# Optimization experiments

Measured on AMD Instinct MI355X. Metric: run time of the kernel, lower is better.

## Reference

```python
import jax, jax.numpy as jnp
import numpy as np

B, T, D, L, N_MELS, MAX_R = 128, 1024, 256, 512, 80, 20

def setup_inputs() -> dict:
    key = jax.random.key(0)
    ks = jax.random.split(key, 40)
    s = 0.05
    inp = {
        'encoder_seq': jax.random.normal(ks[0], (B, T, D), jnp.float32),
        'encoder_seq_proj': jax.random.normal(ks[1], (B, T, D), jnp.float32),
        'prenet_in': jax.random.normal(ks[2], (B, N_MELS), jnp.float32),
        'attn_hidden': jax.random.normal(ks[3], (B, D), jnp.float32),
        'rnn1_hidden': jax.random.normal(ks[4], (B, L), jnp.float32),
        'rnn2_hidden': jax.random.normal(ks[5], (B, L), jnp.float32),
        'rnn1_cell': jax.random.normal(ks[6], (B, L), jnp.float32),
        'rnn2_cell': jax.random.normal(ks[7], (B, L), jnp.float32),
        'context_vec': jax.random.normal(ks[8], (B, D), jnp.float32),
        # PreNet
        'fc1_W': jax.random.normal(ks[9], (256, N_MELS), jnp.float32) * s,
        'fc1_b': jnp.zeros((256,), jnp.float32),
        'fc2_W': jax.random.normal(ks[10], (128, 256), jnp.float32) * s,
        'fc2_b': jnp.zeros((128,), jnp.float32),
        # Attention
        'attn_W': jax.random.normal(ks[11], (D, D), jnp.float32) * s,
        'attn_v': jax.random.normal(ks[12], (1, D), jnp.float32) * s,
        # GRUCell: input size D + D//2 = 384
        'gru_Wih': jax.random.normal(ks[13], (3 * D, D + D // 2), jnp.float32) * s,
        'gru_Whh': jax.random.normal(ks[14], (3 * D, D), jnp.float32) * s,
        'gru_bih': jnp.zeros((3 * D,), jnp.float32),
        'gru_bhh': jnp.zeros((3 * D,), jnp.float32),
        # rnn_input Linear: 2*D -> L
        'rnn_in_W': jax.random.normal(ks[15], (L, 2 * D), jnp.float32) * s,
        'rnn_in_b': jnp.zeros((L,), jnp.float32),
        # LSTMCell 1
        'l1_Wih': jax.random.normal(ks[16], (4 * L, L), jnp.float32) * s,
        'l1_Whh': jax.random.normal(ks[17], (4 * L, L), jnp.float32) * s,
        'l1_bih': jnp.zeros((4 * L,), jnp.float32),
        'l1_bhh': jnp.zeros((4 * L,), jnp.float32),
        # LSTMCell 2
        'l2_Wih': jax.random.normal(ks[18], (4 * L, L), jnp.float32) * s,
        'l2_Whh': jax.random.normal(ks[19], (4 * L, L), jnp.float32) * s,
        'l2_bih': jnp.zeros((4 * L,), jnp.float32),
        'l2_bhh': jnp.zeros((4 * L,), jnp.float32),
        # mel projection (no bias)
        'mel_W': jax.random.normal(ks[20], (N_MELS * MAX_R, L), jnp.float32) * s,
        'r': 2,
    }
    return inp


def _lstm_cell(x, h, c, Wih, Whh, bih, bhh):
    g = x @ Wih.T + bih + h @ Whh.T + bhh
    i, f, gg, o = jnp.split(g, 4, axis=-1)
    c_new = jax.nn.sigmoid(f) * c + jax.nn.sigmoid(i) * jnp.tanh(gg)
    h_new = jax.nn.sigmoid(o) * jnp.tanh(c_new)
    return h_new, c_new


def reference(encoder_seq, encoder_seq_proj, prenet_in, attn_hidden, rnn1_hidden,
              rnn2_hidden, rnn1_cell, rnn2_cell, context_vec,
              fc1_W, fc1_b, fc2_W, fc2_b, attn_W, attn_v,
              gru_Wih, gru_Whh, gru_bih, gru_bhh, rnn_in_W, rnn_in_b,
              l1_Wih, l1_Whh, l1_bih, l1_bhh, l2_Wih, l2_Whh, l2_bih, l2_bhh,
              mel_W, r):
    # PreNet (eval mode: dropout identity)
    p = jax.nn.relu(prenet_in @ fc1_W.T + fc1_b)
    p = jax.nn.relu(p @ fc2_W.T + fc2_b)  # [B, D//2]

    # GRUCell (torch semantics)
    x_in = jnp.concatenate([context_vec, p], axis=-1)  # [B, D + D//2]
    gi = x_in @ gru_Wih.T + gru_bih
    gh = attn_hidden @ gru_Whh.T + gru_bhh
    i_r, i_z, i_n = jnp.split(gi, 3, axis=-1)
    h_r, h_z, h_n = jnp.split(gh, 3, axis=-1)
    rg = jax.nn.sigmoid(i_r + h_r)
    zg = jax.nn.sigmoid(i_z + h_z)
    ng = jnp.tanh(i_n + rg * h_n)
    attn_h = (1.0 - zg) * ng + zg * attn_hidden  # [B, D]

    # Bahdanau attention, softmax over time (dim=1)
    q = attn_h @ attn_W.T  # [B, D]
    u = jnp.tanh(encoder_seq_proj + q[:, None, :]) @ attn_v.T  # [B, T, 1]
    scores = jax.nn.softmax(u, axis=1)
    scores_t = jnp.swapaxes(scores, 1, 2)  # [B, 1, T]
    context = jnp.matmul(scores_t, encoder_seq)[:, 0, :]  # [B, D]

    x = jnp.concatenate([context, attn_h], axis=1) @ rnn_in_W.T + rnn_in_b  # [B, L]

    rnn1_h, rnn1_c = _lstm_cell(x, rnn1_hidden, rnn1_cell, l1_Wih, l1_Whh, l1_bih, l1_bhh)
    x = x + rnn1_h
    rnn2_h, rnn2_c = _lstm_cell(x, rnn2_hidden, rnn2_cell, l2_Wih, l2_Whh, l2_bih, l2_bhh)
    x = x + rnn2_h

    mels = (x @ mel_W.T).reshape(x.shape[0], N_MELS, MAX_R)[:, :, :r]
    return (mels, scores_t, attn_h, rnn1_h, rnn2_h, rnn1_c, rnn2_c, context)
```

## Files before the change

kernel.cpp:

```cpp
#include <hip/hip_runtime.h>
#include <math.h>

#define B_   128
#define T_   1024
#define D_   256
#define L_   512

__device__ __forceinline__ float sigmoidf_(float x) {
    return 1.f / (1.f + __expf(-x));
}
__device__ __forceinline__ float tanhf_(float x) {
    x = fminf(fmaxf(x, -15.f), 15.f);
    float e = __expf(2.f * x);
    return (e - 1.f) / (e + 1.f);
}
__device__ __forceinline__ float tanh_fast(float x) {
    float e = __expf(2.f * x);
    return 1.f - 2.f * __builtin_amdgcn_rcpf(e + 1.f);
}
__device__ __forceinline__ float waveReduceSum(float v) {
    #pragma unroll
    for (int o = 32; o > 0; o >>= 1) v += __shfl_xor(v, o, 64);
    return v;
}
__device__ __forceinline__ float waveReduceMax(float v) {
    #pragma unroll
    for (int o = 32; o > 0; o >>= 1) v = fmaxf(v, __shfl_xor(v, o, 64));
    return v;
}

__global__ __launch_bounds__(256) void k1a_prenet(
    const float* __restrict__ prenet_in,
    const float* __restrict__ fc1_W, const float* __restrict__ fc1_b,
    const float* __restrict__ fc2_W, const float* __restrict__ fc2_b,
    float* __restrict__ p2_out)
{
    const int b = blockIdx.x, t = threadIdx.x;
    __shared__ __align__(16) float pin[80];
    __shared__ __align__(16) float p1[256];

    if (t < 80) pin[t] = prenet_in[b * 80 + t];
    __syncthreads();

    {
        float a = fc1_b[t];
        const float4* w  = (const float4*)(fc1_W + t * 80);
        const float4* xv = (const float4*)pin;
        #pragma unroll
        for (int k = 0; k < 20; k++) {
            float4 wv = w[k], v = xv[k];
            a += v.x * wv.x + v.y * wv.y + v.z * wv.z + v.w * wv.w;
        }
        p1[t] = fmaxf(a, 0.f);
    }
    __syncthreads();

    if (t < 128) {
        float a = fc2_b[t];
        const float4* w  = (const float4*)(fc2_W + t * 256);
        const float4* xv = (const float4*)p1;
        #pragma unroll 8
        for (int k = 0; k < 64; k++) {
            float4 wv = w[k], v = xv[k];
            a += v.x * wv.x + v.y * wv.y + v.z * wv.z + v.w * wv.w;
        }
        p2_out[b * 128 + t] = fmaxf(a, 0.f);
    }
}

__global__ __launch_bounds__(256) void k1b_gru_gemv(
    const float* __restrict__ context_vec, const float* __restrict__ p2,
    const float* __restrict__ attn_hidden,
    const float* __restrict__ gru_Wih, const float* __restrict__ gru_Whh,
    const float* __restrict__ gru_bih, const float* __restrict__ gru_bhh,
    float* __restrict__ gi_out, float* __restrict__ gh_out)
{
    const int t = threadIdx.x;
    const int j = blockIdx.x * 256 + t;
    const int b0 = blockIdx.y * 2;

    __shared__ __align__(16) float xs[2][384];
    __shared__ __align__(16) float hs[2][256];

    for (int i = t; i < 768; i += 256) {
        int bb = i / 384, k = i % 384;
        xs[bb][k] = (k < 256) ? context_vec[(b0 + bb) * 256 + k]
                              : p2[(b0 + bb) * 128 + (k - 256)];
    }
    for (int i = t; i < 512; i += 256) {
        hs[i / 256][i % 256] = attn_hidden[(b0 + i / 256) * 256 + (i % 256)];
    }
    __syncthreads();

    {
        float a0 = gru_bih[j], a1 = a0;
        const float4* w  = (const float4*)(gru_Wih + (size_t)j * 384);
        const float4* x0 = (const float4*)xs[0];
        const float4* x1 = (const float4*)xs[1];
        #pragma unroll 8
        for (int k = 0; k < 96; k++) {
            float4 wv = w[k], v0 = x0[k], v1 = x1[k];
            a0 += v0.x * wv.x + v0.y * wv.y + v0.z * wv.z + v0.w * wv.w;
            a1 += v1.x * wv.x + v1.y * wv.y + v1.z * wv.z + v1.w * wv.w;
        }
        gi_out[(size_t)(b0 + 0) * 768 + j] = a0;
        gi_out[(size_t)(b0 + 1) * 768 + j] = a1;
    }
    {
        float a0 = gru_bhh[j], a1 = a0;
        const float4* w  = (const float4*)(gru_Whh + (size_t)j * 256);
        const float4* x0 = (const float4*)hs[0];
        const float4* x1 = (const float4*)hs[1];
        #pragma unroll 8
        for (int k = 0; k < 64; k++) {
            float4 wv = w[k], v0 = x0[k], v1 = x1[k];
            a0 += v0.x * wv.x + v0.y * wv.y + v0.z * wv.z + v0.w * wv.w;
            a1 += v1.x * wv.x + v1.y * wv.y + v1.z * wv.z + v1.w * wv.w;
        }
        gh_out[(size_t)(b0 + 0) * 768 + j] = a0;
        gh_out[(size_t)(b0 + 1) * 768 + j] = a1;
    }
}

__global__ __launch_bounds__(256) void k1c_gates_q(
    const float* __restrict__ gi, const float* __restrict__ gh,
    const float* __restrict__ attn_hidden, const float* __restrict__ attn_W,
    float* __restrict__ attn_h_out, float* __restrict__ q_out)
{
    const int b = blockIdx.x, t = threadIdx.x;
    __shared__ __align__(16) float ahn[256];

    {
        float hp = attn_hidden[b * 256 + t];
        float rg = sigmoidf_(gi[(size_t)b * 768 + t]       + gh[(size_t)b * 768 + t]);
        float zg = sigmoidf_(gi[(size_t)b * 768 + 256 + t] + gh[(size_t)b * 768 + 256 + t]);
        float ng = tanhf_(gi[(size_t)b * 768 + 512 + t] + rg * gh[(size_t)b * 768 + 512 + t]);
        float h  = (1.f - zg) * ng + zg * hp;
        ahn[t] = h;
        attn_h_out[b * 256 + t] = h;
    }
    __syncthreads();

    {
        float a = 0.f;
        const float4* w  = (const float4*)(attn_W + (size_t)t * 256);
        const float4* xv = (const float4*)ahn;
        #pragma unroll 8
        for (int k = 0; k < 64; k++) {
            float4 wv = w[k], v = xv[k];
            a += v.x * wv.x + v.y * wv.y + v.z * wv.z + v.w * wv.w;
        }
        q_out[b * 256 + t] = a;
    }
}

__global__ __launch_bounds__(256) void ka_attn(
    const float* __restrict__ enc_proj, const float* __restrict__ enc,
    const float* __restrict__ q, const float* __restrict__ v,
    float* __restrict__ u_out, float* __restrict__ ctx_part,
    float* __restrict__ m_part, float* __restrict__ s_part)
{
    const int b     = blockIdx.x >> 4;
    const int chunk = blockIdx.x & 15;
    const int tid   = threadIdx.x;
    const int lane  = tid & 63;
    const int wv    = tid >> 6;
    const int g     = lane >> 4;
    const int gl    = lane & 15;

    __shared__ float ul[64];
    __shared__ float el[64];
    __shared__ __align__(16) float4 red[4][64];

    const int t0 = chunk * 64;

    float4 qv[4], vv[4];
    #pragma unroll
    for (int c = 0; c < 4; c++) {
        qv[c] = ((const float4*)(q + b * 256))[c * 16 + gl];
        vv[c] = ((const float4*)v)[c * 16 + gl];
    }

    const float* ebase = enc_proj + ((size_t)(b * T_ + t0)) * 256;
    #pragma unroll
    for (int pass = 0; pass < 4; pass++) {
        const int t = wv * 16 + pass * 4 + g;
        const float4* row = (const float4*)(ebase + (size_t)t * 256);
        float s = 0.f;
        #pragma unroll
        for (int c = 0; c < 4; c++) {
            float4 pj = row[c * 16 + gl];
            s += tanh_fast(pj.x + qv[c].x) * vv[c].x
               + tanh_fast(pj.y + qv[c].y) * vv[c].y
               + tanh_fast(pj.z + qv[c].z) * vv[c].z
               + tanh_fast(pj.w + qv[c].w) * vv[c].w;
        }
        s += __shfl_xor(s, 1, 64);
        s += __shfl_xor(s, 2, 64);
        s += __shfl_xor(s, 4, 64);
        s += __shfl_xor(s, 8, 64);
        if (gl == 0) ul[t] = s;
    }
    __syncthreads();

    if (wv == 0) {
        float x = ul[lane];
        u_out[b * T_ + t0 + lane] = x;
        float mx = waveReduceMax(x);
        float e = __expf(x - mx);
        el[lane] = e;
        float ss = waveReduceSum(e);
        if (lane == 0) {
            m_part[b * 16 + chunk] = mx;
            s_part[b * 16 + chunk] = ss;
        }
    }
    __syncthreads();

    const float4* base2 = (const float4*)(enc + ((size_t)(b * T_ + t0)) * 256);
    float4 acc0 = {0.f, 0.f, 0.f, 0.f}, acc1 = {0.f, 0.f, 0.f, 0.f};
    #pragma unroll
    for (int i = 0; i < 16; i += 2) {
        int t = wv * 16 + i;
        float e0 = el[t], e1 = el[t + 1];
        float4 v0 = base2[(size_t)t * 64 + lane];
        float4 v1 = base2[(size_t)(t + 1) * 64 + lane];
        acc0.x += e0 * v0.x; acc0.y += e0 * v0.y; acc0.z += e0 * v0.z; acc0.w += e0 * v0.w;
        acc1.x += e1 * v1.x; acc1.y += e1 * v1.y; acc1.z += e1 * v1.z; acc1.w += e1 * v1.w;
    }
    acc0.x += acc1.x; acc0.y += acc1.y; acc0.z += acc1.z; acc0.w += acc1.w;
    red[wv][lane] = acc0;
    __syncthreads();
    if (tid < 64) {
        float4 s = red[0][tid];
        float4 a1 = red[1][tid], a2 = red[2][tid], a3 = red[3][tid];
        s.x += a1.x + a2.x + a3.x;
        s.y += a1.y + a2.y + a3.y;
        s.z += a1.z + a2.z + a3.z;
        s.w += a1.w + a2.w + a3.w;
        ((float4*)ctx_part)[(size_t)(b * 16 + chunk) * 64 + tid] = s;
    }
}

__global__ __launch_bounds__(256) void kb_combine(
    const float* __restrict__ u, const float* __restrict__ m_part,
    const float* __restrict__ s_part, const float* __restrict__ ctx_part,
    const float* __restrict__ attn_h,
    float* __restrict__ scores_out, float* __restrict__ ctx_out,
    float* __restrict__ concat1)
{
    const int b = blockIdx.x, tid = threadIdx.x;
    __shared__ float msh[16], ssh[16];
    if (tid < 16) {
        msh[tid] = m_part[b * 16 + tid];
        ssh[tid] = s_part[b * 16 + tid];
    }
    __syncthreads();

    float M = msh[0];
    #pragma unroll
    for (int c = 1; c < 16; c++) M = fmaxf(M, msh[c]);
    float S = 0.f;
    #pragma unroll
    for (int c = 0; c < 16; c++) S += ssh[c] * __expf(msh[c] - M);
    float invS = 1.f / S;

    {
        float a = 0.f;
        #pragma unroll
        for (int c = 0; c < 16; c++)
            a += ctx_part[(size_t)(b * 16 + c) * 256 + tid] * __expf(msh[c] - M);
        a *= invS;
        ctx_out[b * 256 + tid] = a;
        concat1[b * 512 + tid] = a;
        concat1[b * 512 + 256 + tid] = attn_h[b * 256 + tid];
    }

    #pragma unroll
    for (int i = 0; i < 4; i++) {
        int t = i * 256 + tid;
        scores_out[b * T_ + t] = __expf(u[b * T_ + t] - M) * invS;
    }
}

__global__ __launch_bounds__(256) void gemm512_splitk(
    const float* __restrict__ A1, const float* __restrict__ W1,
    const float* __restrict__ A2, const float* __restrict__ W2,
    float* __restrict__ part, int N, int ksPerSeg)
{
    const int n0 = blockIdx.x * 64, m0 = blockIdx.y * 64;
    const int seg = blockIdx.z / ksPerSeg, ls = blockIdx.z % ksPerSeg;
    const int KSZ = 512 / ksPerSeg;
    const float* A = seg ? A2 : A1;
    const float* W = seg ? W2 : W1;
    const int k0 = ls * KSZ;

    __shared__ __align__(16) float As[32][68];
    __shared__ __align__(16) float Ws[32][68];

    const int tid = threadIdx.x;
    const int tm = tid & 15, tn = tid >> 4;
    const int rs = tid >> 3, qs = tid & 7;

    float acc[4][4] = {};

    for (int kt = 0; kt < KSZ; kt += 32) {
        #pragma unroll
        for (int it = 0; it < 2; it++) {
            int r = rs + it * 32;
            float4 av = *(const float4*)(A + (size_t)(m0 + r) * 512 + k0 + kt + qs * 4);
            As[qs * 4 + 0][r] = av.x; As[qs * 4 + 1][r] = av.y;
            As[qs * 4 + 2][r] = av.z; As[qs * 4 + 3][r] = av.w;
            float4 wv = *(const float4*)(W + (size_t)(n0 + r) * 512 + k0 + kt + qs * 4);
            Ws[qs * 4 + 0][r] = wv.x; Ws[qs * 4 + 1][r] = wv.y;
            Ws[qs * 4 + 2][r] = wv.z; Ws[qs * 4 + 3][r] = wv.w;
        }
        __syncthreads();
        #pragma unroll
        for (int kk = 0; kk < 32; kk++) {
            float4 a = *(const float4*)&As[kk][tm * 4];
            float4 w = *(const float4*)&Ws[kk][tn * 4];
            acc[0][0] += a.x * w.x; acc[0][1] += a.x * w.y; acc[0][2] += a.x * w.z; acc[0][3] += a.x * w.w;
            acc[1][0] += a.y * w.x; acc[1][1] += a.y * w.y; acc[1][2] += a.y * w.z; acc[1][3] += a.y * w.w;
            acc[2][0] += a.z * w.x; acc[2][1] += a.z * w.y; acc[2][2] += a.z * w.z; acc[2][3] += a.z * w.w;
            acc[3][0] += a.w * w.x; acc[3][1] += a.w * w.y; acc[3][2] += a.w * w.z; acc[3][3] += a.w * w.w;
        }
        __syncthreads();
    }

    float* pb = part + ((size_t)blockIdx.z * 128 + m0) * N + n0;
    #pragma unroll
    for (int i = 0; i < 4; i++) {
        float4 o = {acc[i][0], acc[i][1], acc[i][2], acc[i][3]};
        *(float4*)(pb + (size_t)(tm * 4 + i) * N + tn * 4) = o;
    }
}

__global__ __launch_bounds__(256) void e_rnn(
    const float* __restrict__ part, const float* __restrict__ bias,
    float* __restrict__ x)
{
    const int idx = blockIdx.x * 256 + threadIdx.x;
    const int n = idx & 511;
    float a = bias[n];
    #pragma unroll
    for (int z = 0; z < 4; z++) a += part[(size_t)z * 65536 + idx];
    x[idx] = a;
}

__global__ __launch_bounds__(256) void e_lstm(
    const float* __restrict__ part,
    const float* __restrict__ bih, const float* __restrict__ bhh,
    const float* __restrict__ c_prev, const float* __restrict__ x_prev,
    float* __restrict__ h_out, float* __restrict__ c_out, float* __restrict__ x_new)
{
    const int idx = blockIdx.x * 256 + threadIdx.x;
    const int bb = idx >> 9, j = idx & 511;
    float gi = bih[j] + bhh[j];
    float gf = bih[512 + j] + bhh[512 + j];
    float gg = bih[1024 + j] + bhh[1024 + j];
    float go = bih[1536 + j] + bhh[1536 + j];
    #pragma unroll
    for (int z = 0; z < 4; z++) {
        const float* p = part + ((size_t)z * 128 + bb) * 2048;
        gi += p[j]; gf += p[512 + j]; gg += p[1024 + j]; go += p[1536 + j];
    }
    float c = sigmoidf_(gf) * c_prev[idx] + sigmoidf_(gi) * tanhf_(gg);
    float h = sigmoidf_(go) * tanhf_(c);
    h_out[idx] = h;
    c_out[idx] = c;
    x_new[idx] = x_prev[idx] + h;
}

__global__ __launch_bounds__(512) void e_lstm2_mel(
    const float* __restrict__ part,
    const float* __restrict__ bih, const float* __restrict__ bhh,
    const float* __restrict__ c_prev, const float* __restrict__ x_prev,
    const float* __restrict__ mel_W, const int* __restrict__ r_ptr,
    float* __restrict__ h_out, float* __restrict__ c_out,
    float* __restrict__ mels)
{
    const int b = blockIdx.x, j = threadIdx.x;
    __shared__ __align__(16) float xs[512];

    const int idx = b * 512 + j;
    float gi = bih[j] + bhh[j];
    float gf = bih[512 + j] + bhh[512 + j];
    float gg = bih[1024 + j] + bhh[1024 + j];
    float go = bih[1536 + j] + bhh[1536 + j];
    #pragma unroll
    for (int z = 0; z < 4; z++) {
        const float* p = part + ((size_t)z * 128 + b) * 2048;
        gi += p[j]; gf += p[512 + j]; gg += p[1024 + j]; go += p[1536 + j];
    }
    float c = sigmoidf_(gf) * c_prev[idx] + sigmoidf_(gi) * tanhf_(gg);
    float h = sigmoidf_(go) * tanhf_(c);
    h_out[idx] = h;
    c_out[idx] = c;
    xs[j] = x_prev[idx] + h;
    __syncthreads();

    const int r = r_ptr[0];
    const int tot = 80 * r;
    for (int n = j; n < tot; n += 512) {
        int m = n / r, rr = n % r;
        const float4* w  = (const float4*)(mel_W + (size_t)(m * 20 + rr) * 512);
        const float4* xv = (const float4*)xs;
        float a = 0.f;
        #pragma unroll 8
        for (int k = 0; k < 128; k++) {
            float4 wv = w[k], vv = xv[k];
            a += wv.x * vv.x + wv.y * vv.y + wv.z * vv.z + wv.w * vv.w;
        }
        mels[(size_t)b * tot + n] = a;
    }
}

extern "C" void kernel_launch(void* const* d_in, const int* in_sizes, int n_in,
                              void* d_out, int out_size, void* d_ws, size_t ws_size,
                              hipStream_t stream)
{
    const float* enc   = (const float*)d_in[0];
    const float* encp  = (const float*)d_in[1];
    const float* pre   = (const float*)d_in[2];
    const float* ah_in = (const float*)d_in[3];
    const float* r1h   = (const float*)d_in[4];
    const float* r2h   = (const float*)d_in[5];
    const float* r1c   = (const float*)d_in[6];
    const float* r2c   = (const float*)d_in[7];
    const float* cvec  = (const float*)d_in[8];
    const float* fc1W  = (const float*)d_in[9];
    const float* fc1b  = (const float*)d_in[10];
    const float* fc2W  = (const float*)d_in[11];
    const float* fc2b  = (const float*)d_in[12];
    const float* attnW = (const float*)d_in[13];
    const float* attnv = (const float*)d_in[14];
    const float* gWih  = (const float*)d_in[15];
    const float* gWhh  = (const float*)d_in[16];
    const float* gbih  = (const float*)d_in[17];
    const float* gbhh  = (const float*)d_in[18];
    const float* rinW  = (const float*)d_in[19];
    const float* rinb  = (const float*)d_in[20];
    const float* l1Wih = (const float*)d_in[21];
    const float* l1Whh = (const float*)d_in[22];
    const float* l1bih = (const float*)d_in[23];
    const float* l1bhh = (const float*)d_in[24];
    const float* l2Wih = (const float*)d_in[25];
    const float* l2Whh = (const float*)d_in[26];
    const float* l2bih = (const float*)d_in[27];
    const float* l2bhh = (const float*)d_in[28];
    const float* melW  = (const float*)d_in[29];
    const int*   rp    = (const int*)d_in[30];

    float* out = (float*)d_out;
    float* o_mels  = out + 0;
    float* o_scor  = out + 20480;
    float* o_attnh = out + 151552;
    float* o_r1h   = out + 184320;
    float* o_r2h   = out + 249856;
    float* o_r1c   = out + 315392;
    float* o_r2c   = out + 380928;
    float* o_ctx   = out + 446464;

    float* ws     = (float*)d_ws;
    float* w_q    = ws + 0;
    float* w_u    = ws + 32768;
    float* w_m    = ws + 163840;
    float* w_s    = ws + 165888;
    float* w_ctxp = ws + 167936;
    float* w_cat1 = ws + 692224;
    float* w_x    = ws + 757760;
    float* w_x2   = ws + 823296;
    float* w_part = ws + 888832;

    float* w_p2 = w_part;
    float* w_gi = w_part + 16384;
    float* w_gh = w_part + 114688;

    hipLaunchKernelGGL(k1a_prenet, dim3(128), dim3(256), 0, stream,
                       pre, fc1W, fc1b, fc2W, fc2b, w_p2);

    hipLaunchKernelGGL(k1b_gru_gemv, dim3(3, 64), dim3(256), 0, stream,
                       cvec, w_p2, ah_in, gWih, gWhh, gbih, gbhh, w_gi, w_gh);

    hipLaunchKernelGGL(k1c_gates_q, dim3(128), dim3(256), 0, stream,
                       w_gi, w_gh, ah_in, attnW, o_attnh, w_q);

    hipLaunchKernelGGL(ka_attn, dim3(2048), dim3(256), 0, stream,
                       encp, enc, w_q, attnv, w_u, w_ctxp, w_m, w_s);

    hipLaunchKernelGGL(kb_combine, dim3(128), dim3(256), 0, stream,
                       w_u, w_m, w_s, w_ctxp, o_attnh, o_scor, o_ctx, w_cat1);

    hipLaunchKernelGGL(gemm512_splitk, dim3(8, 2, 4), dim3(256), 0, stream,
                       w_cat1, rinW, w_cat1, rinW, w_part, 512, 4);
    hipLaunchKernelGGL(e_rnn, dim3(256), dim3(256), 0, stream, w_part, rinb, w_x);

    hipLaunchKernelGGL(gemm512_splitk, dim3(32, 2, 4), dim3(256), 0, stream,
                       w_x, l1Wih, r1h, l1Whh, w_part, 2048, 2);
    hipLaunchKernelGGL(e_lstm, dim3(256), dim3(256), 0, stream,
                       w_part, l1bih, l1bhh, r1c, w_x, o_r1h, o_r1c, w_x2);

    hipLaunchKernelGGL(gemm512_splitk, dim3(32, 2, 4), dim3(256), 0, stream,
                       w_x2, l2Wih, r2h, l2Whh, w_part, 2048, 2);
    hipLaunchKernelGGL(e_lstm2_mel, dim3(128), dim3(512), 0, stream,
                       w_part, l2bih, l2bhh, r2c, w_x2, melW, rp,
                       o_r2h, o_r2c, o_mels);
}
```

Before: 155.1 us.

## Fuse prenet into GRU gemv, prefetch encoder rows, raise split-K to 16

The prenet MLP now runs inside the GRU input GEMV kernel, removing one launch and the p2 round trip through global memory, at the cost of recomputing the prenet in each of the three column blocks. The attention kernel gets a minimum-occupancy launch bound and prefetches half of the encoder rows for the context sum before the softmax barrier, overlapping those loads with the reduction. The three split-K GEMMs go from 4 to 16 K-splits for more parallelism, and their epilogues now sum 16 partial buffers. Larger split-K adds partial-sum traffic and workspace use, and the prefetch raises register pressure.

```diff
diff --git a/kernel.cpp b/kernel.cpp
--- a/kernel.cpp
+++ b/kernel.cpp
@@ -29,66 +29,58 @@
     return v;
 }
 
-__global__ __launch_bounds__(256) void k1a_prenet(
-    const float* __restrict__ prenet_in,
+__global__ __launch_bounds__(256) void k1b_fused(
+    const float* __restrict__ prenet_in, const float* __restrict__ context_vec,
+    const float* __restrict__ attn_hidden,
     const float* __restrict__ fc1_W, const float* __restrict__ fc1_b,
     const float* __restrict__ fc2_W, const float* __restrict__ fc2_b,
-    float* __restrict__ p2_out)
-{
-    const int b = blockIdx.x, t = threadIdx.x;
-    __shared__ __align__(16) float pin[80];
-    __shared__ __align__(16) float p1[256];
-
-    if (t < 80) pin[t] = prenet_in[b * 80 + t];
-    __syncthreads();
-
-    {
-        float a = fc1_b[t];
+    const float* __restrict__ gru_Wih, const float* __restrict__ gru_Whh,
+    const float* __restrict__ gru_bih, const float* __restrict__ gru_bhh,
+    float* __restrict__ gi_out, float* __restrict__ gh_out)
+{
+    const int t = threadIdx.x;
+    const int j = blockIdx.x * 256 + t;
+    const int b0 = blockIdx.y * 2;
+
+    __shared__ __align__(16) float pin[2][80];
+    __shared__ __align__(16) float p1[2][256];
+    __shared__ __align__(16) float xs[2][384];
+    __shared__ __align__(16) float hs[2][256];
+
+    if (t < 160) pin[t / 80][t % 80] = prenet_in[(b0 + t / 80) * 80 + (t % 80)];
+    xs[0][t] = context_vec[b0 * 256 + t];
+    xs[1][t] = context_vec[(b0 + 1) * 256 + t];
+    hs[0][t] = attn_hidden[b0 * 256 + t];
+    hs[1][t] = attn_hidden[(b0 + 1) * 256 + t];
+    __syncthreads();
+
+    {
+        float a0 = fc1_b[t], a1 = a0;
         const float4* w  = (const float4*)(fc1_W + t * 80);
-        const float4* xv = (const float4*)pin;
+        const float4* x0 = (const float4*)pin[0];
+        const float4* x1 = (const float4*)pin[1];
         #pragma unroll
         for (int k = 0; k < 20; k++) {
-            float4 wv = w[k], v = xv[k];
-            a += v.x * wv.x + v.y * wv.y + v.z * wv.z + v.w * wv.w;
-        }
-        p1[t] = fmaxf(a, 0.f);
-    }
-    __syncthreads();
-
-    if (t < 128) {
-        float a = fc2_b[t];
-        const float4* w  = (const float4*)(fc2_W + t * 256);
-        const float4* xv = (const float4*)p1;
+            float4 wv = w[k], v0 = x0[k], v1 = x1[k];
+            a0 += v0.x * wv.x + v0.y * wv.y + v0.z * wv.z + v0.w * wv.w;
+            a1 += v1.x * wv.x + v1.y * wv.y + v1.z * wv.z + v1.w * wv.w;
+        }
+        p1[0][t] = fmaxf(a0, 0.f);
+        p1[1][t] = fmaxf(a1, 0.f);
+    }
+    __syncthreads();
+
+    {
+        const int bb = t >> 7, jj = t & 127;
+        float a = fc2_b[jj];
+        const float4* w  = (const float4*)(fc2_W + jj * 256);
+        const float4* xv = (const float4*)p1[bb];
         #pragma unroll 8
         for (int k = 0; k < 64; k++) {
             float4 wv = w[k], v = xv[k];
             a += v.x * wv.x + v.y * wv.y + v.z * wv.z + v.w * wv.w;
         }
-        p2_out[b * 128 + t] = fmaxf(a, 0.f);
-    }
-}
-
-__global__ __launch_bounds__(256) void k1b_gru_gemv(
-    const float* __restrict__ context_vec, const float* __restrict__ p2,
-    const float* __restrict__ attn_hidden,
-    const float* __restrict__ gru_Wih, const float* __restrict__ gru_Whh,
-    const float* __restrict__ gru_bih, const float* __restrict__ gru_bhh,
-    float* __restrict__ gi_out, float* __restrict__ gh_out)
-{
-    const int t = threadIdx.x;
-    const int j = blockIdx.x * 256 + t;
-    const int b0 = blockIdx.y * 2;
-
-    __shared__ __align__(16) float xs[2][384];
-    __shared__ __align__(16) float hs[2][256];
-
-    for (int i = t; i < 768; i += 256) {
-        int bb = i / 384, k = i % 384;
-        xs[bb][k] = (k < 256) ? context_vec[(b0 + bb) * 256 + k]
-                              : p2[(b0 + bb) * 128 + (k - 256)];
-    }
-    for (int i = t; i < 512; i += 256) {
-        hs[i / 256][i % 256] = attn_hidden[(b0 + i / 256) * 256 + (i % 256)];
+        xs[bb][256 + jj] = fmaxf(a, 0.f);
     }
     __syncthreads();
 
@@ -154,7 +146,7 @@
     }
 }
 
-__global__ __launch_bounds__(256) void ka_attn(
+__global__ __launch_bounds__(256, 4) void ka_attn(
     const float* __restrict__ enc_proj, const float* __restrict__ enc,
     const float* __restrict__ q, const float* __restrict__ v,
     float* __restrict__ u_out, float* __restrict__ ctx_part,
@@ -201,6 +193,13 @@
         s += __shfl_xor(s, 8, 64);
         if (gl == 0) ul[t] = s;
     }
+
+    const float4* base2 = (const float4*)(enc + ((size_t)(b * T_ + t0)) * 256);
+    float4 pre[8];
+    #pragma unroll
+    for (int i = 0; i < 8; i++)
+        pre[i] = base2[(size_t)(wv * 16 + i) * 64 + lane];
+
     __syncthreads();
 
     if (wv == 0) {
@@ -217,10 +216,17 @@
     }
     __syncthreads();
 
-    const float4* base2 = (const float4*)(enc + ((size_t)(b * T_ + t0)) * 256);
     float4 acc0 = {0.f, 0.f, 0.f, 0.f}, acc1 = {0.f, 0.f, 0.f, 0.f};
     #pragma unroll
-    for (int i = 0; i < 16; i += 2) {
+    for (int i = 0; i < 8; i += 2) {
+        float e0 = el[wv * 16 + i], e1 = el[wv * 16 + i + 1];
+        acc0.x += e0 * pre[i].x;     acc0.y += e0 * pre[i].y;
+        acc0.z += e0 * pre[i].z;     acc0.w += e0 * pre[i].w;
+        acc1.x += e1 * pre[i + 1].x; acc1.y += e1 * pre[i + 1].y;
+        acc1.z += e1 * pre[i + 1].z; acc1.w += e1 * pre[i + 1].w;
+    }
+    #pragma unroll
+    for (int i = 8; i < 16; i += 2) {
         int t = wv * 16 + i;
         float e0 = el[t], e1 = el[t + 1];
         float4 v0 = base2[(size_t)t * 64 + lane];
@@ -344,7 +350,7 @@
     const int n = idx & 511;
     float a = bias[n];
     #pragma unroll
-    for (int z = 0; z < 4; z++) a += part[(size_t)z * 65536 + idx];
+    for (int z = 0; z < 16; z++) a += part[(size_t)z * 65536 + idx];
     x[idx] = a;
 }
 
@@ -361,7 +367,7 @@
     float gg = bih[1024 + j] + bhh[1024 + j];
     float go = bih[1536 + j] + bhh[1536 + j];
     #pragma unroll
-    for (int z = 0; z < 4; z++) {
+    for (int z = 0; z < 16; z++) {
         const float* p = part + ((size_t)z * 128 + bb) * 2048;
         gi += p[j]; gf += p[512 + j]; gg += p[1024 + j]; go += p[1536 + j];
     }
@@ -389,7 +395,7 @@
     float gg = bih[1024 + j] + bhh[1024 + j];
     float go = bih[1536 + j] + bhh[1536 + j];
     #pragma unroll
-    for (int z = 0; z < 4; z++) {
+    for (int z = 0; z < 16; z++) {
         const float* p = part + ((size_t)z * 128 + b) * 2048;
         gi += p[j]; gf += p[512 + j]; gg += p[1024 + j]; go += p[1536 + j];
     }
@@ -473,15 +479,12 @@
     float* w_x2   = ws + 823296;
     float* w_part = ws + 888832;
 
-    float* w_p2 = w_part;
-    float* w_gi = w_part + 16384;
-    float* w_gh = w_part + 114688;
-
-    hipLaunchKernelGGL(k1a_prenet, dim3(128), dim3(256), 0, stream,
-                       pre, fc1W, fc1b, fc2W, fc2b, w_p2);
-
-    hipLaunchKernelGGL(k1b_gru_gemv, dim3(3, 64), dim3(256), 0, stream,
-                       cvec, w_p2, ah_in, gWih, gWhh, gbih, gbhh, w_gi, w_gh);
+    float* w_gi = w_part;
+    float* w_gh = w_part + 98304;
+
+    hipLaunchKernelGGL(k1b_fused, dim3(3, 64), dim3(256), 0, stream,
+                       pre, cvec, ah_in, fc1W, fc1b, fc2W, fc2b,
+                       gWih, gWhh, gbih, gbhh, w_gi, w_gh);
 
     hipLaunchKernelGGL(k1c_gates_q, dim3(128), dim3(256), 0, stream,
                        w_gi, w_gh, ah_in, attnW, o_attnh, w_q);
@@ -492,17 +495,17 @@
     hipLaunchKernelGGL(kb_combine, dim3(128), dim3(256), 0, stream,
                        w_u, w_m, w_s, w_ctxp, o_attnh, o_scor, o_ctx, w_cat1);
 
-    hipLaunchKernelGGL(gemm512_splitk, dim3(8, 2, 4), dim3(256), 0, stream,
-                       w_cat1, rinW, w_cat1, rinW, w_part, 512, 4);
+    hipLaunchKernelGGL(gemm512_splitk, dim3(8, 2, 16), dim3(256), 0, stream,
+                       w_cat1, rinW, w_cat1, rinW, w_part, 512, 16);
     hipLaunchKernelGGL(e_rnn, dim3(256), dim3(256), 0, stream, w_part, rinb, w_x);
 
-    hipLaunchKernelGGL(gemm512_splitk, dim3(32, 2, 4), dim3(256), 0, stream,
-                       w_x, l1Wih, r1h, l1Whh, w_part, 2048, 2);
+    hipLaunchKernelGGL(gemm512_splitk, dim3(32, 2, 16), dim3(256), 0, stream,
+                       w_x, l1Wih, r1h, l1Whh, w_part, 2048, 8);
     hipLaunchKernelGGL(e_lstm, dim3(256), dim3(256), 0, stream,
                        w_part, l1bih, l1bhh, r1c, w_x, o_r1h, o_r1c, w_x2);
 
-    hipLaunchKernelGGL(gemm512_splitk, dim3(32, 2, 4), dim3(256), 0, stream,
-                       w_x2, l2Wih, r2h, l2Whh, w_part, 2048, 2);
+    hipLaunchKernelGGL(gemm512_splitk, dim3(32, 2, 16), dim3(256), 0, stream,
+                       w_x2, l2Wih, r2h, l2Whh, w_part, 2048, 8);
     hipLaunchKernelGGL(e_lstm2_mel, dim3(128), dim3(512), 0, stream,
                        w_part, l2bih, l2bhh, r2c, w_x2, melW, rp,
                        o_r2h, o_r2c, o_mels);
```

Result: faster. 147.6 us (-4.8%).
